# Optimization experiments

Measured on AMD Instinct MI355X. Metric: run time of the kernel, lower is better.

The kernel has to match this reference:

```python
import jax, jax.numpy as jnp
import numpy as np

N_NODES = 100000
N_EDGES = 600000
IN_C, HID_C, OUT_C = 128, 128, 64


def gcn_conv(x, W, b, src, dst, n_nodes):
    """PyG GCNConv: out = D^{-1/2} (A + I) D^{-1/2} X W + b (symmetric norm, self-loops)."""
    h = x @ W  # [N, C_out] transform first (as PyG does)
    # add self loops
    loop = jnp.arange(n_nodes, dtype=src.dtype)
    s = jnp.concatenate([src, loop])
    d = jnp.concatenate([dst, loop])
    # degree over targets (edge weight = 1)
    deg = jax.ops.segment_sum(jnp.ones_like(d, dtype=h.dtype), d, num_segments=n_nodes)
    dinv = jnp.where(deg > 0, jax.lax.rsqrt(deg), 0.0)
    norm = dinv[s] * dinv[d]  # [E+N]
    msg = h[s] * norm[:, None]  # gather + scale
    out = jax.ops.segment_sum(msg, d, num_segments=n_nodes)  # scatter-add
    return out + b


def setup_inputs() -> dict:
    key = jax.random.key(0)
    k1, k2, k3, k4, k5 = jax.random.split(key, 5)
    x = jax.random.normal(k1, (N_NODES, IN_C), dtype=jnp.float32)
    src = jax.random.randint(k2, (N_EDGES,), 0, N_NODES, dtype=jnp.int32)
    dst = jax.random.randint(k3, (N_EDGES,), 0, N_NODES, dtype=jnp.int32)
    # Glorot-style init for conv weights, zero bias (PyG defaults)
    W1 = jax.random.normal(k4, (IN_C, HID_C), dtype=jnp.float32) * (1.0 / np.sqrt(IN_C))
    W2 = jax.random.normal(k5, (HID_C, OUT_C), dtype=jnp.float32) * (1.0 / np.sqrt(HID_C))
    b1 = jnp.zeros((HID_C,), dtype=jnp.float32)
    b2 = jnp.zeros((OUT_C,), dtype=jnp.float32)
    return {"x": x, "W1": W1, "b1": b1, "W2": W2, "b2": b2, "src": src, "dst": dst}


def reference(x, W1, b1, W2, b2, src, dst):
    h = gcn_conv(x, W1, b1, src, dst, N_NODES)
    h = jax.nn.relu(h)
    out = gcn_conv(h, W2, b2, src, dst, N_NODES)
    return out
```

## Files before the change

kernel.cpp:

```cpp
#include <hip/hip_runtime.h>
#include <math.h>


typedef __bf16 bf16x8 __attribute__((ext_vector_type(8)));
typedef float f32x4 __attribute__((ext_vector_type(4)));

constexpr int CAP = 32;
constexpr int CAPB = 8192;

union ABu {
  unsigned short u16[8];
  uint4 u4;
  bf16x8 v;
};

__device__ inline unsigned short f2bf(float f) {
  unsigned u = __float_as_uint(f);
  return (unsigned short)((u + 0x7fffu + ((u >> 16) & 1u)) >> 16);
}

__device__ inline void unpack8(uint4 v, float* f) {
  f[0] = __uint_as_float(v.x << 16);
  f[1] = __uint_as_float(v.x & 0xffff0000u);
  f[2] = __uint_as_float(v.y << 16);
  f[3] = __uint_as_float(v.y & 0xffff0000u);
  f[4] = __uint_as_float(v.z << 16);
  f[5] = __uint_as_float(v.z & 0xffff0000u);
  f[6] = __uint_as_float(v.w << 16);
  f[7] = __uint_as_float(v.w & 0xffff0000u);
}

__device__ inline uint4 pack8(const float* a) {
  uint4 o;
  o.x = (unsigned)f2bf(a[0]) | ((unsigned)f2bf(a[1]) << 16);
  o.y = (unsigned)f2bf(a[2]) | ((unsigned)f2bf(a[3]) << 16);
  o.z = (unsigned)f2bf(a[4]) | ((unsigned)f2bf(a[5]) << 16);
  o.w = (unsigned)f2bf(a[6]) | ((unsigned)f2bf(a[7]) << 16);
  return o;
}

__global__ __launch_bounds__(256) void k_pre(const float* __restrict__ W1,
                                             const float* __restrict__ W2,
                                             unsigned short* __restrict__ Wb1,
                                             unsigned short* __restrict__ Wb2,
                                             int* __restrict__ gCur, int nbins) {
  constexpr int CONV_BLOCKS = (128 * 128 + 128 * 64) / 256;
  if (blockIdx.x == CONV_BLOCKS) {
    if ((int)threadIdx.x < nbins) gCur[threadIdx.x] = 0;
    return;
  }
  int idx = blockIdx.x * 256 + threadIdx.x;
  if (idx < 128 * 128) {
    int k = idx >> 7, c = idx & 127;
    Wb1[(((k >> 3) << 7) + c) * 8 + (k & 7)] = f2bf(W1[idx]);
  } else {
    int j = idx - 128 * 128;
    int k = j >> 6, c = j & 63;
    Wb2[(((k >> 3) << 6) + c) * 8 + (k & 7)] = f2bf(W2[j]);
  }
}


__device__ inline void binA_body(const int* __restrict__ src,
                                 const int* __restrict__ dst,
                                 int* __restrict__ gCur,
                                 int2* __restrict__ binBuf,
                                 int E, int nbins, int bid,
                                 int* bc, int* bbase) {
  const int tid = threadIdx.x;
  if (tid < 128) bc[tid] = 0;
  __syncthreads();
  int base = (bid * 256 + tid) * 8;
  int ds[8], ss[8];
  bool vl[8];
  if (base + 7 < E) {
    int4 d0 = *(const int4*)(dst + base);
    int4 d1 = *(const int4*)(dst + base + 4);
    int4 s0 = *(const int4*)(src + base);
    int4 s1 = *(const int4*)(src + base + 4);
    ds[0] = d0.x; ds[1] = d0.y; ds[2] = d0.z; ds[3] = d0.w;
    ds[4] = d1.x; ds[5] = d1.y; ds[6] = d1.z; ds[7] = d1.w;
    ss[0] = s0.x; ss[1] = s0.y; ss[2] = s0.z; ss[3] = s0.w;
    ss[4] = s1.x; ss[5] = s1.y; ss[6] = s1.z; ss[7] = s1.w;
#pragma unroll
    for (int i = 0; i < 8; ++i) vl[i] = true;
  } else {
#pragma unroll
    for (int i = 0; i < 8; ++i) {
      int e = base + i;
      bool v = e < E;
      int ee = v ? e : E - 1;
      ds[i] = dst[ee]; ss[i] = src[ee]; vl[i] = v;
    }
  }
#pragma unroll
  for (int i = 0; i < 8; ++i)
    if (vl[i]) atomicAdd(&bc[ds[i] >> 10], 1);
  __syncthreads();
  if (tid < nbins) bbase[tid] = atomicAdd(&gCur[tid], bc[tid]);
  __syncthreads();
  if (tid < 128) bc[tid] = 0;
  __syncthreads();
#pragma unroll
  for (int i = 0; i < 8; ++i) {
    if (vl[i]) {
      int b = ds[i] >> 10;
      int pos = bbase[b] + atomicAdd(&bc[b], 1);
      if (pos < CAPB) binBuf[(size_t)b * CAPB + pos] = make_int2(ss[i], ds[i]);
    }
  }
}

__device__ inline void gemm1_body(const float* __restrict__ X,
                                  const unsigned short* __restrict__ Wb,
                                  unsigned short* __restrict__ Cb, int M,
                                  int rowblk) {
  constexpr int K = 128, N = 128, NT = N / 16, KS = K / 32;
  const int tid = threadIdx.x;
  const int wave = tid >> 6;
  const int lane = tid & 63;
  const int q = lane >> 4;
  const int l15 = lane & 15;
  const int row0 = rowblk * 64 + wave * 16;
  const int rowA = row0 + l15;

  f32x4 zero = {0.0f, 0.0f, 0.0f, 0.0f};
  f32x4 acc[NT];
#pragma unroll
  for (int t = 0; t < NT; ++t) acc[t] = zero;

#pragma unroll
  for (int kk = 0; kk < KS; ++kk) {
    ABu a;
    float4 f0 = make_float4(0.f, 0.f, 0.f, 0.f);
    float4 f1 = make_float4(0.f, 0.f, 0.f, 0.f);
    if (rowA < M) {
      const float4* ap = (const float4*)(X + (size_t)rowA * K + kk * 32 + q * 8);
      f0 = ap[0];
      f1 = ap[1];
    }
    a.u16[0] = f2bf(f0.x); a.u16[1] = f2bf(f0.y);
    a.u16[2] = f2bf(f0.z); a.u16[3] = f2bf(f0.w);
    a.u16[4] = f2bf(f1.x); a.u16[5] = f2bf(f1.y);
    a.u16[6] = f2bf(f1.z); a.u16[7] = f2bf(f1.w);
#pragma unroll
    for (int nt = 0; nt < NT; ++nt) {
      ABu b;
      b.u4 = *(const uint4*)(Wb + ((size_t)(kk * 4 + q) * N + nt * 16 + l15) * 8);
      acc[nt] = __builtin_amdgcn_mfma_f32_16x16x32_bf16(a.v, b.v, acc[nt], 0, 0, 0);
    }
  }

#pragma unroll
  for (int v = 0; v < 4; ++v) {
    int row = row0 + q * 4 + v;
    if (row < M) {
#pragma unroll
      for (int nt = 0; nt < NT; ++nt)
        Cb[(size_t)row * N + nt * 16 + l15] = f2bf(acc[nt][v]);
    }
  }
}

__global__ __launch_bounds__(256) void k_binA_gemm1(
    const int* __restrict__ src, const int* __restrict__ dst,
    int* __restrict__ gCur, int2* __restrict__ binBuf, int E, int nbins,
    int EB, const float* __restrict__ X, const unsigned short* __restrict__ Wb1,
    unsigned short* __restrict__ h1, int M) {
  __shared__ int bc[128];
  __shared__ int bbase[128];
  if ((int)blockIdx.x < EB)
    binA_body(src, dst, gCur, binBuf, E, nbins, blockIdx.x, bc, bbase);
  else
    gemm1_body(X, Wb1, h1, M, blockIdx.x - EB);
}

__global__ __launch_bounds__(256) void k_binB(const int2* __restrict__ binBuf,
                                              const int* __restrict__ gCur,
                                              int* __restrict__ counts,
                                              float* __restrict__ dinv,
                                              int* __restrict__ eslot, int N) {
  __shared__ int hist[1024];
  const int b = blockIdx.x;
  const int base = b << 10;
  int lim = N - base;
  lim = lim < 1024 ? lim : 1024;
  for (int i = threadIdx.x; i < 1024; i += 256) hist[i] = 0;
  __syncthreads();
  int cnt = gCur[b];
  cnt = cnt < CAPB ? cnt : CAPB;
  const int2* bb = binBuf + (size_t)b * CAPB;
  for (int i = threadIdx.x; i < cnt; i += 256) {
    int2 pr = bb[i];
    int rk = atomicAdd(&hist[pr.y - base], 1);
    rk = rk < CAP - 1 ? rk : CAP - 1;
    eslot[(size_t)pr.y * CAP + rk] = pr.x;
  }
  __syncthreads();
  for (int i = threadIdx.x; i < lim; i += 256) {
    int c = hist[i];
    counts[base + i] = c;
    dinv[base + i] = rsqrtf((float)(c + 1));
  }
}

__global__ __launch_bounds__(256) void k_aggemm(const unsigned short* __restrict__ h1,
                                                const float* __restrict__ dinv,
                                                const float* __restrict__ b1,
                                                const int* __restrict__ counts,
                                                const int* __restrict__ eslot,
                                                const unsigned short* __restrict__ Wb2,
                                                unsigned short* __restrict__ h2s,
                                                int n) {
  constexpr int LDA = 136;
  __shared__ unsigned short As[16 * LDA];
  __shared__ float sdinv[16];
  const int tid = threadIdx.x;

  {
    const int nl = tid >> 4;
    const int q = tid & 15;
    const int node = blockIdx.x * 16 + nl;
    float acc[8];
    if (node < n) {
      const uint4* h4 = (const uint4*)h1;
      float di = dinv[node];
      if (q == 0) sdinv[nl] = di;
      unpack8(h4[(size_t)node * 16 + q], acc);
#pragma unroll
      for (int j = 0; j < 8; ++j) acc[j] *= di;

      int cnt = counts[node];
      if (cnt > CAP) cnt = CAP;
      const int* sl = eslot + (size_t)node * CAP;
      if (cnt > 0) {
        int lim = cnt < 16 ? cnt : 16;
        int my_s = sl[q < lim ? q : 0];
        if ((unsigned)my_s >= (unsigned)n) my_s = 0;
        float my_dv = dinv[my_s];
        for (int e = 0; e < lim; e += 8) {
          int idx[8];
          float dv[8];
#pragma unroll
          for (int i = 0; i < 8; ++i) {
            idx[i] = __shfl(my_s, e + i, 16);
            float dl = __shfl(my_dv, e + i, 16);
            dv[i] = (e + i < lim) ? dl : 0.f;
          }
          uint4 rr[8];
#pragma unroll
          for (int i = 0; i < 8; ++i) rr[i] = h4[(size_t)idx[i] * 16 + q];
#pragma unroll
          for (int i = 0; i < 8; ++i) {
            float g[8];
            unpack8(rr[i], g);
#pragma unroll
            for (int j = 0; j < 8; ++j) acc[j] = fmaf(g[j], dv[i], acc[j]);
          }
        }
        if (cnt > 16) {
          int rem = cnt - 16;
          int my_s2 = sl[16 + (q < rem ? q : 0)];
          if ((unsigned)my_s2 >= (unsigned)n) my_s2 = 0;
          float my_dv2 = dinv[my_s2];
          for (int e = 0; e < rem; e += 8) {
            int idx[8];
            float dv[8];
#pragma unroll
            for (int i = 0; i < 8; ++i) {
              idx[i] = __shfl(my_s2, e + i, 16);
              float dl = __shfl(my_dv2, e + i, 16);
              dv[i] = (e + i < rem) ? dl : 0.f;
            }
            uint4 rr[8];
#pragma unroll
            for (int i = 0; i < 8; ++i) rr[i] = h4[(size_t)idx[i] * 16 + q];
#pragma unroll
            for (int i = 0; i < 8; ++i) {
              float g[8];
              unpack8(rr[i], g);
#pragma unroll
              for (int j = 0; j < 8; ++j) acc[j] = fmaf(g[j], dv[i], acc[j]);
            }
          }
        }
      }
      const float4* b14 = (const float4*)b1;
      float4 ba = b14[q * 2], bb = b14[q * 2 + 1];
      float bias[8] = {ba.x, ba.y, ba.z, ba.w, bb.x, bb.y, bb.z, bb.w};
#pragma unroll
      for (int i = 0; i < 8; ++i) acc[i] = fmaxf(fmaf(acc[i], di, bias[i]), 0.f);
    } else {
      if (q == 0) sdinv[nl] = 0.f;
#pragma unroll
      for (int i = 0; i < 8; ++i) acc[i] = 0.f;
    }
    *(uint4*)&As[nl * LDA + q * 8] = pack8(acc);
  }
  __syncthreads();

  {
    const int wave = tid >> 6;
    const int lane = tid & 63;
    const int q = lane >> 4;
    const int l15 = lane & 15;
    f32x4 acc = {0.0f, 0.0f, 0.0f, 0.0f};
#pragma unroll
    for (int kk = 0; kk < 4; ++kk) {
      ABu a, b;
      a.u4 = *(const uint4*)&As[l15 * LDA + kk * 32 + q * 8];
      b.u4 = *(const uint4*)(Wb2 + ((size_t)(kk * 4 + q) * 64 + wave * 16 + l15) * 8);
      acc = __builtin_amdgcn_mfma_f32_16x16x32_bf16(a.v, b.v, acc, 0, 0, 0);
    }
#pragma unroll
    for (int v = 0; v < 4; ++v) {
      int rl = q * 4 + v;
      int row = blockIdx.x * 16 + rl;
      if (row < n) h2s[(size_t)row * 64 + wave * 16 + l15] = f2bf(acc[v] * sdinv[rl]);
    }
  }
}

__global__ __launch_bounds__(256) void k_agg2(const unsigned short* __restrict__ h2s,
                                              const float* __restrict__ dinv,
                                              const float* __restrict__ b2,
                                              const int* __restrict__ counts,
                                              const int* __restrict__ eslot,
                                              float* __restrict__ out, int n) {
  constexpr int CQ = 8;
  const int tid = threadIdx.x;
  const int node = blockIdx.x * 32 + tid / CQ;
  const int q = tid % CQ;
  if (node >= n) return;

  const uint4* h4 = (const uint4*)h2s;
  float di = dinv[node];
  float acc[8];
  unpack8(h4[(size_t)node * CQ + q], acc);

  int cnt = counts[node];
  if (cnt > CAP) cnt = CAP;
  const int* sl = eslot + (size_t)node * CAP;
  for (int b = 0; b * 8 < cnt; ++b) {
    int rem = cnt - b * 8;
    int lim = rem < 8 ? rem : 8;
    int my_s = sl[b * 8 + (q < lim ? q : 0)];
    if ((unsigned)my_s >= (unsigned)n) my_s = 0;
    int idx[8];
#pragma unroll
    for (int i = 0; i < 8; ++i) idx[i] = __shfl(my_s, i, 8);
    uint4 rr[8];
#pragma unroll
    for (int i = 0; i < 8; ++i) rr[i] = h4[(size_t)idx[i] * CQ + q];
#pragma unroll
    for (int i = 0; i < 8; ++i) {
      float w = (i < lim) ? 1.f : 0.f;
      float g[8];
      unpack8(rr[i], g);
#pragma unroll
      for (int j = 0; j < 8; ++j) acc[j] = fmaf(g[j], w, acc[j]);
    }
  }

  const float4* b24 = (const float4*)b2;
  float4 ba = b24[q * 2], bb = b24[q * 2 + 1];
  float bias[8] = {ba.x, ba.y, ba.z, ba.w, bb.x, bb.y, bb.z, bb.w};
  float4 o0, o1;
  o0.x = fmaf(acc[0], di, bias[0]);
  o0.y = fmaf(acc[1], di, bias[1]);
  o0.z = fmaf(acc[2], di, bias[2]);
  o0.w = fmaf(acc[3], di, bias[3]);
  o1.x = fmaf(acc[4], di, bias[4]);
  o1.y = fmaf(acc[5], di, bias[5]);
  o1.z = fmaf(acc[6], di, bias[6]);
  o1.w = fmaf(acc[7], di, bias[7]);
  ((float4*)out)[(size_t)node * 16 + q * 2 + 0] = o0;
  ((float4*)out)[(size_t)node * 16 + q * 2 + 1] = o1;
}


extern "C" void kernel_launch(void* const* d_in, const int* in_sizes, int n_in,
                              void* d_out, int out_size, void* d_ws, size_t ws_size,
                              hipStream_t stream) {
  const float* x  = (const float*)d_in[0];
  const float* W1 = (const float*)d_in[1];
  const float* b1 = (const float*)d_in[2];
  const float* W2 = (const float*)d_in[3];
  const float* b2 = (const float*)d_in[4];
  const int* src  = (const int*)d_in[5];
  const int* dst  = (const int*)d_in[6];
  float* out = (float*)d_out;

  constexpr int IN_C = 128, HID_C = 128, OUT_C = 64;
  const int N = in_sizes[0] / IN_C;
  const int E = in_sizes[5];
  const int nbins = (N + 1023) >> 10;

  char* p = (char*)d_ws;
  auto alloc = [&](size_t bytes) {
    char* r = p;
    p += (bytes + 255) & ~(size_t)255;
    return r;
  };
  int*   gCur    = (int*)alloc((size_t)nbins * 4);
  int2*  binBuf  = (int2*)alloc((size_t)nbins * CAPB * 8);
  float* dinv    = (float*)alloc((size_t)N * 4);
  int*   counts  = (int*)alloc((size_t)N * 4);
  int*   eslot   = (int*)alloc((size_t)N * CAP * 4);
  unsigned short* Wb1 = (unsigned short*)alloc((size_t)IN_C * HID_C * 2);
  unsigned short* Wb2 = (unsigned short*)alloc((size_t)HID_C * OUT_C * 2);
  unsigned short* h1  = (unsigned short*)alloc((size_t)N * HID_C * 2);
  unsigned short* h2s = (unsigned short*)alloc((size_t)N * OUT_C * 2);

  const int T = 256;
  const int EB8 = ((E + 7) / 8 + T - 1) / T;
  const int RB_TOTAL = (N + 63) / 64;
  constexpr int CONV_BLOCKS = (128 * 128 + 128 * 64) / 256;

  k_pre<<<CONV_BLOCKS + 1, T, 0, stream>>>(W1, W2, Wb1, Wb2, gCur, nbins);
  k_binA_gemm1<<<EB8 + RB_TOTAL, T, 0, stream>>>(src, dst, gCur, binBuf, E, nbins,
                                                 EB8, x, Wb1, h1, N);
  k_binB<<<nbins, T, 0, stream>>>(binBuf, gCur, counts, dinv, eslot, N);
  k_aggemm<<<(N + 15) / 16, T, 0, stream>>>(h1, dinv, b1, counts, eslot, Wb2, h2s, N);
  k_agg2<<<(N + 31) / 32, T, 0, stream>>>(h2s, dinv, b2, counts, eslot, out, N);
}
```

Before: 188.3 us.

## Shrink destination bins and build per-block neighbor lists in shared memory

Destination bins shrink from 1024 to 256 nodes, and the global per-node eslot/counts CSR is dropped. k_binB now only counts degrees to compute dinv. Each aggregation block rescans its whole 256-node bin (about 1.5K edge pairs) and builds its own local neighbor slots in shared memory. This removes the scattered eslot writes and reads, at the cost of every block re-reading the full bin, which is 16x redundancy for aggemm and 8x for agg2.

After: 206.2 us. +9.5%, slower.

```diff
diff --git a/kernel.cpp b/kernel.cpp
--- a/kernel.cpp
+++ b/kernel.cpp
@@ -6,7 +6,8 @@
 typedef float f32x4 __attribute__((ext_vector_type(4)));
 
 constexpr int CAP = 32;
-constexpr int CAPB = 8192;
+constexpr int BIN_SHIFT = 8;
+constexpr int CAPB = 2048;
 
 union ABu {
   unsigned short u16[8];
@@ -46,7 +47,7 @@
                                              int* __restrict__ gCur, int nbins) {
   constexpr int CONV_BLOCKS = (128 * 128 + 128 * 64) / 256;
   if (blockIdx.x == CONV_BLOCKS) {
-    if ((int)threadIdx.x < nbins) gCur[threadIdx.x] = 0;
+    for (int i = threadIdx.x; i < nbins; i += 256) gCur[i] = 0;
     return;
   }
   int idx = blockIdx.x * 256 + threadIdx.x;
@@ -68,7 +69,7 @@
                                  int E, int nbins, int bid,
                                  int* bc, int* bbase) {
   const int tid = threadIdx.x;
-  if (tid < 128) bc[tid] = 0;
+  for (int i = tid; i < nbins; i += 256) bc[i] = 0;
   __syncthreads();
   int base = (bid * 256 + tid) * 8;
   int ds[8], ss[8];
@@ -95,16 +96,19 @@
   }
 #pragma unroll
   for (int i = 0; i < 8; ++i)
-    if (vl[i]) atomicAdd(&bc[ds[i] >> 10], 1);
-  __syncthreads();
-  if (tid < nbins) bbase[tid] = atomicAdd(&gCur[tid], bc[tid]);
-  __syncthreads();
-  if (tid < 128) bc[tid] = 0;
+    if (vl[i]) atomicAdd(&bc[ds[i] >> BIN_SHIFT], 1);
+  __syncthreads();
+  for (int i = tid; i < nbins; i += 256) {
+    int c = bc[i];
+    bbase[i] = c ? atomicAdd(&gCur[i], c) : 0;
+  }
+  __syncthreads();
+  for (int i = tid; i < nbins; i += 256) bc[i] = 0;
   __syncthreads();
 #pragma unroll
   for (int i = 0; i < 8; ++i) {
     if (vl[i]) {
-      int b = ds[i] >> 10;
+      int b = ds[i] >> BIN_SHIFT;
       int pos = bbase[b] + atomicAdd(&bc[b], 1);
       if (pos < CAPB) binBuf[(size_t)b * CAPB + pos] = make_int2(ss[i], ds[i]);
     }
@@ -167,8 +171,8 @@
     int* __restrict__ gCur, int2* __restrict__ binBuf, int E, int nbins,
     int EB, const float* __restrict__ X, const unsigned short* __restrict__ Wb1,
     unsigned short* __restrict__ h1, int M) {
-  __shared__ int bc[128];
-  __shared__ int bbase[128];
+  __shared__ int bc[512];
+  __shared__ int bbase[512];
   if ((int)blockIdx.x < EB)
     binA_body(src, dst, gCur, binBuf, E, nbins, blockIdx.x, bc, bbase);
   else
@@ -177,50 +181,62 @@
 
 __global__ __launch_bounds__(256) void k_binB(const int2* __restrict__ binBuf,
                                               const int* __restrict__ gCur,
-                                              int* __restrict__ counts,
-                                              float* __restrict__ dinv,
-                                              int* __restrict__ eslot, int N) {
-  __shared__ int hist[1024];
+                                              float* __restrict__ dinv, int N) {
+  __shared__ int hist[256];
   const int b = blockIdx.x;
-  const int base = b << 10;
+  const int base = b << BIN_SHIFT;
   int lim = N - base;
-  lim = lim < 1024 ? lim : 1024;
-  for (int i = threadIdx.x; i < 1024; i += 256) hist[i] = 0;
+  lim = lim < 256 ? lim : 256;
+  if ((int)threadIdx.x < 256) hist[threadIdx.x] = 0;
   __syncthreads();
   int cnt = gCur[b];
   cnt = cnt < CAPB ? cnt : CAPB;
   const int2* bb = binBuf + (size_t)b * CAPB;
-  for (int i = threadIdx.x; i < cnt; i += 256) {
-    int2 pr = bb[i];
-    int rk = atomicAdd(&hist[pr.y - base], 1);
-    rk = rk < CAP - 1 ? rk : CAP - 1;
-    eslot[(size_t)pr.y * CAP + rk] = pr.x;
-  }
-  __syncthreads();
-  for (int i = threadIdx.x; i < lim; i += 256) {
-    int c = hist[i];
-    counts[base + i] = c;
-    dinv[base + i] = rsqrtf((float)(c + 1));
-  }
+  for (int i = threadIdx.x; i < cnt; i += 256)
+    atomicAdd(&hist[bb[i].y - base], 1);
+  __syncthreads();
+  if ((int)threadIdx.x < lim)
+    dinv[base + threadIdx.x] = rsqrtf((float)(hist[threadIdx.x] + 1));
 }
 
 __global__ __launch_bounds__(256) void k_aggemm(const unsigned short* __restrict__ h1,
                                                 const float* __restrict__ dinv,
                                                 const float* __restrict__ b1,
-                                                const int* __restrict__ counts,
-                                                const int* __restrict__ eslot,
+                                                const int* __restrict__ gCur,
+                                                const int2* __restrict__ binBuf,
                                                 const unsigned short* __restrict__ Wb2,
                                                 unsigned short* __restrict__ h2s,
                                                 int n) {
   constexpr int LDA = 136;
   __shared__ unsigned short As[16 * LDA];
   __shared__ float sdinv[16];
+  __shared__ int lhist[16];
+  __shared__ int lslot[16 * CAP];
   const int tid = threadIdx.x;
+  const int base16 = blockIdx.x * 16;
+
+  {
+    if (tid < 16) lhist[tid] = 0;
+    __syncthreads();
+    const int bin = base16 >> BIN_SHIFT;
+    int cnt = gCur[bin];
+    cnt = cnt < CAPB ? cnt : CAPB;
+    const int2* bb = binBuf + (size_t)bin * CAPB;
+    for (int i = tid; i < cnt; i += 256) {
+      int2 pr = bb[i];
+      unsigned loc = (unsigned)(pr.y - base16);
+      if (loc < 16u) {
+        int rk = atomicAdd(&lhist[loc], 1);
+        if (rk < CAP) lslot[loc * CAP + rk] = pr.x;
+      }
+    }
+    __syncthreads();
+  }
 
   {
     const int nl = tid >> 4;
     const int q = tid & 15;
-    const int node = blockIdx.x * 16 + nl;
+    const int node = base16 + nl;
     float acc[8];
     if (node < n) {
       const uint4* h4 = (const uint4*)h1;
@@ -230,13 +246,12 @@
 #pragma unroll
       for (int j = 0; j < 8; ++j) acc[j] *= di;
 
-      int cnt = counts[node];
+      int cnt = lhist[nl];
       if (cnt > CAP) cnt = CAP;
-      const int* sl = eslot + (size_t)node * CAP;
+      const int* sl = &lslot[nl * CAP];
       if (cnt > 0) {
         int lim = cnt < 16 ? cnt : 16;
         int my_s = sl[q < lim ? q : 0];
-        if ((unsigned)my_s >= (unsigned)n) my_s = 0;
         float my_dv = dinv[my_s];
         for (int e = 0; e < lim; e += 8) {
           int idx[8];
@@ -261,7 +276,6 @@
         if (cnt > 16) {
           int rem = cnt - 16;
           int my_s2 = sl[16 + (q < rem ? q : 0)];
-          if ((unsigned)my_s2 >= (unsigned)n) my_s2 = 0;
           float my_dv2 = dinv[my_s2];
           for (int e = 0; e < rem; e += 8) {
             int idx[8];
@@ -315,7 +329,7 @@
 #pragma unroll
     for (int v = 0; v < 4; ++v) {
       int rl = q * 4 + v;
-      int row = blockIdx.x * 16 + rl;
+      int row = base16 + rl;
       if (row < n) h2s[(size_t)row * 64 + wave * 16 + l15] = f2bf(acc[v] * sdinv[rl]);
     }
   }
@@ -324,12 +338,34 @@
 __global__ __launch_bounds__(256) void k_agg2(const unsigned short* __restrict__ h2s,
                                               const float* __restrict__ dinv,
                                               const float* __restrict__ b2,
-                                              const int* __restrict__ counts,
-                                              const int* __restrict__ eslot,
+                                              const int* __restrict__ gCur,
+                                              const int2* __restrict__ binBuf,
                                               float* __restrict__ out, int n) {
   constexpr int CQ = 8;
+  __shared__ int lhist[32];
+  __shared__ int lslot[32 * CAP];
   const int tid = threadIdx.x;
-  const int node = blockIdx.x * 32 + tid / CQ;
+  const int base32 = blockIdx.x * 32;
+
+  {
+    if (tid < 32) lhist[tid] = 0;
+    __syncthreads();
+    const int bin = base32 >> BIN_SHIFT;
+    int cnt = gCur[bin];
+    cnt = cnt < CAPB ? cnt : CAPB;
+    const int2* bb = binBuf + (size_t)bin * CAPB;
+    for (int i = tid; i < cnt; i += 256) {
+      int2 pr = bb[i];
+      unsigned loc = (unsigned)(pr.y - base32);
+      if (loc < 32u) {
+        int rk = atomicAdd(&lhist[loc], 1);
+        if (rk < CAP) lslot[loc * CAP + rk] = pr.x;
+      }
+    }
+    __syncthreads();
+  }
+
+  const int node = base32 + tid / CQ;
   const int q = tid % CQ;
   if (node >= n) return;
 
@@ -338,14 +374,13 @@
   float acc[8];
   unpack8(h4[(size_t)node * CQ + q], acc);
 
-  int cnt = counts[node];
+  int cnt = lhist[tid / CQ];
   if (cnt > CAP) cnt = CAP;
-  const int* sl = eslot + (size_t)node * CAP;
+  const int* sl = &lslot[(tid / CQ) * CAP];
   for (int b = 0; b * 8 < cnt; ++b) {
     int rem = cnt - b * 8;
     int lim = rem < 8 ? rem : 8;
     int my_s = sl[b * 8 + (q < lim ? q : 0)];
-    if ((unsigned)my_s >= (unsigned)n) my_s = 0;
     int idx[8];
 #pragma unroll
     for (int i = 0; i < 8; ++i) idx[i] = __shfl(my_s, i, 8);
@@ -394,7 +429,7 @@
   constexpr int IN_C = 128, HID_C = 128, OUT_C = 64;
   const int N = in_sizes[0] / IN_C;
   const int E = in_sizes[5];
-  const int nbins = (N + 1023) >> 10;
+  const int nbins = (N + 255) >> BIN_SHIFT;
 
   char* p = (char*)d_ws;
   auto alloc = [&](size_t bytes) {
@@ -405,8 +440,6 @@
   int*   gCur    = (int*)alloc((size_t)nbins * 4);
   int2*  binBuf  = (int2*)alloc((size_t)nbins * CAPB * 8);
   float* dinv    = (float*)alloc((size_t)N * 4);
-  int*   counts  = (int*)alloc((size_t)N * 4);
-  int*   eslot   = (int*)alloc((size_t)N * CAP * 4);
   unsigned short* Wb1 = (unsigned short*)alloc((size_t)IN_C * HID_C * 2);
   unsigned short* Wb2 = (unsigned short*)alloc((size_t)HID_C * OUT_C * 2);
   unsigned short* h1  = (unsigned short*)alloc((size_t)N * HID_C * 2);
@@ -420,7 +453,7 @@
   k_pre<<<CONV_BLOCKS + 1, T, 0, stream>>>(W1, W2, Wb1, Wb2, gCur, nbins);
   k_binA_gemm1<<<EB8 + RB_TOTAL, T, 0, stream>>>(src, dst, gCur, binBuf, E, nbins,
                                                  EB8, x, Wb1, h1, N);
-  k_binB<<<nbins, T, 0, stream>>>(binBuf, gCur, counts, dinv, eslot, N);
-  k_aggemm<<<(N + 15) / 16, T, 0, stream>>>(h1, dinv, b1, counts, eslot, Wb2, h2s, N);
-  k_agg2<<<(N + 31) / 32, T, 0, stream>>>(h2s, dinv, b2, counts, eslot, out, N);
-}
+  k_binB<<<nbins, T, 0, stream>>>(binBuf, gCur, dinv, N);
+  k_aggemm<<<(N + 15) / 16, T, 0, stream>>>(h1, dinv, b1, gCur, binBuf, Wb2, h2s, N);
+  k_agg2<<<(N + 31) / 32, T, 0, stream>>>(h2s, dinv, b2, gCur, binBuf, out, N);
+}
```
